# Optimization experiments

Hardware: AMD Instinct MI355X
Metric: run time of the kernel (lower is better)

Reference implementation:

```python
import jax, jax.numpy as jnp
from jax import lax
import numpy as np

EPS_BN = 1e-5
COMMIT = 0.25


def _conv(x, w, b, stride):
    # torch Conv2d(k=3, stride, padding=1); w: (O,I,3,3)
    y = lax.conv_general_dilated(x, w, (stride, stride), ((1, 1), (1, 1)),
                                 dimension_numbers=('NCHW', 'OIHW', 'NCHW'))
    return y + b[None, :, None, None]


def _deconv(x, w, b):
    # torch ConvTranspose2d(k=3, stride=2, padding=1, output_padding=1); w: (I,O,3,3)
    wt = jnp.flip(w, (2, 3)).transpose(1, 0, 2, 3)  # -> (O,I,3,3), spatially flipped
    y = lax.conv_general_dilated(x, wt, (1, 1), ((1, 2), (1, 2)),
                                 lhs_dilation=(2, 2),
                                 dimension_numbers=('NCHW', 'OIHW', 'NCHW'))
    return y + b[None, :, None, None]


def _bn(x, g, b, m, v):
    # eval-mode BatchNorm2d over channel dim 1
    scale = g * lax.rsqrt(v + EPS_BN)
    return (x - m[None, :, None, None]) * scale[None, :, None, None] + b[None, :, None, None]


def _lrelu(x):
    return jax.nn.leaky_relu(x, 0.1)


def _vq(z, emb):
    # z: [B,C,H,W]; emb: [K,C]
    z_nhwc = z.transpose(0, 2, 3, 1)
    B, H, W, C = z_nhwc.shape
    K = emb.shape[0]
    f = z_nhwc.reshape(-1, C)  # [N,C]
    # squared euclidean distances [N,K] without materializing differences
    d = (jnp.sum(f * f, axis=1, keepdims=True)
         - 2.0 * (f @ emb.T)
         + jnp.sum(emb * emb, axis=1)[None, :])
    idx = jnp.argmin(d, axis=1)  # [N]
    q = emb[idx].reshape(B, H, W, C)
    e_latent_loss = jnp.mean((lax.stop_gradient(q) - z_nhwc) ** 2)
    q_latent_loss = jnp.mean((q - lax.stop_gradient(z_nhwc)) ** 2)
    loss = q_latent_loss + COMMIT * e_latent_loss
    q_st = z_nhwc + lax.stop_gradient(q - z_nhwc)  # straight-through
    counts = jnp.zeros((K,), f.dtype).at[idx].add(1.0)
    avg_probs = counts / f.shape[0]
    perplexity = jnp.exp(-jnp.sum(avg_probs * jnp.log(avg_probs + 1e-10)))
    return q_st.transpose(0, 3, 1, 2), loss, perplexity


def reference(x, enc_w1, enc_b1, bn1_g, bn1_b, bn1_m, bn1_v,
              enc_w2, enc_b2, bn2_g, bn2_b, bn2_m, bn2_v,
              enc_w3, enc_b3, bn3_g, bn3_b, bn3_m, bn3_v,
              emb,
              dec_w1, dec_b1, dbn1_g, dbn1_b, dbn1_m, dbn1_v,
              dec_w2, dec_b2, dbn2_g, dbn2_b, dbn2_m, dbn2_v,
              dec_w3, dec_b3):
    # encoder
    h = _lrelu(_bn(_conv(x, enc_w1, enc_b1, 2), bn1_g, bn1_b, bn1_m, bn1_v))
    h = _lrelu(_bn(_conv(h, enc_w2, enc_b2, 2), bn2_g, bn2_b, bn2_m, bn2_v))
    z = _bn(_conv(h, enc_w3, enc_b3, 1), bn3_g, bn3_b, bn3_m, bn3_v)
    # vector quantization
    z_q, vq_loss, perplexity = _vq(z, emb)
    # decoder
    h = _lrelu(_bn(_deconv(z_q, dec_w1, dec_b1), dbn1_g, dbn1_b, dbn1_m, dbn1_v))
    h = _lrelu(_bn(_deconv(h, dec_w2, dec_b2), dbn2_g, dbn2_b, dbn2_m, dbn2_v))
    x_recon = jax.nn.sigmoid(_conv(h, dec_w3, dec_b3, 1))
    return (x_recon, vq_loss, perplexity)


def setup_inputs() -> dict:
    key = jax.random.key(0)
    ks = jax.random.split(key, 10)
    B, Hh, Ww = 32, 256, 256
    C_lat, K = 10, 256
    s = 0.05
    d = {
        'x': jax.random.normal(ks[0], (B, 3, Hh, Ww), jnp.float32),
        'enc_w1': jax.random.normal(ks[1], (32, 3, 3, 3), jnp.float32) * s,
        'enc_b1': jnp.zeros((32,), jnp.float32),
        'bn1_g': jnp.ones((32,), jnp.float32), 'bn1_b': jnp.zeros((32,), jnp.float32),
        'bn1_m': jnp.zeros((32,), jnp.float32), 'bn1_v': jnp.ones((32,), jnp.float32),
        'enc_w2': jax.random.normal(ks[2], (64, 32, 3, 3), jnp.float32) * s,
        'enc_b2': jnp.zeros((64,), jnp.float32),
        'bn2_g': jnp.ones((64,), jnp.float32), 'bn2_b': jnp.zeros((64,), jnp.float32),
        'bn2_m': jnp.zeros((64,), jnp.float32), 'bn2_v': jnp.ones((64,), jnp.float32),
        'enc_w3': jax.random.normal(ks[3], (C_lat, 64, 3, 3), jnp.float32) * s,
        'enc_b3': jnp.zeros((C_lat,), jnp.float32),
        'bn3_g': jnp.ones((C_lat,), jnp.float32), 'bn3_b': jnp.zeros((C_lat,), jnp.float32),
        'bn3_m': jnp.zeros((C_lat,), jnp.float32), 'bn3_v': jnp.ones((C_lat,), jnp.float32),
        'emb': jax.random.uniform(ks[4], (K, C_lat), jnp.float32, -1.0, 1.0),
        'dec_w1': jax.random.normal(ks[5], (C_lat, 64, 3, 3), jnp.float32) * s,
        'dec_b1': jnp.zeros((64,), jnp.float32),
        'dbn1_g': jnp.ones((64,), jnp.float32), 'dbn1_b': jnp.zeros((64,), jnp.float32),
        'dbn1_m': jnp.zeros((64,), jnp.float32), 'dbn1_v': jnp.ones((64,), jnp.float32),
        'dec_w2': jax.random.normal(ks[6], (64, 32, 3, 3), jnp.float32) * s,
        'dec_b2': jnp.zeros((32,), jnp.float32),
        'dbn2_g': jnp.ones((32,), jnp.float32), 'dbn2_b': jnp.zeros((32,), jnp.float32),
        'dbn2_m': jnp.zeros((32,), jnp.float32), 'dbn2_v': jnp.ones((32,), jnp.float32),
        'dec_w3': jax.random.normal(ks[7], (3, 32, 3, 3), jnp.float32) * s,
        'dec_b3': jnp.zeros((3,), jnp.float32),
    }
    return d
```

## Files before the change

### kernel.cpp

```cpp
#include <hip/hip_runtime.h>
#include <hip/hip_bf16.h>
#include <math.h>

typedef __attribute__((ext_vector_type(8))) short bf8v;
typedef __attribute__((ext_vector_type(4))) float f4v;
typedef const __hip_bfloat16* cbfp;

__device__ __forceinline__ void ld4f(const float* p, float* o) {
    float4 t = *(const float4*)p; o[0] = t.x; o[1] = t.y; o[2] = t.z; o[3] = t.w;
}

__global__ __launch_bounds__(256, 2)
void conv1_k(const float* __restrict__ x, const float* __restrict__ w,
             const float* __restrict__ bconv,
             const float* __restrict__ bg, const float* __restrict__ bb,
             const float* __restrict__ bm, const float* __restrict__ bv,
             __hip_bfloat16* __restrict__ out)
{
    __shared__ float sw[3 * 8 * 12];
    int b  = blockIdx.x;
    int yt = b & 15;
    int cg = (b >> 4) & 3;
    int n  = b >> 6;
    int co0 = cg * 8;
    int tid = threadIdx.x;
    for (int idx = tid; idx < 3 * 8 * 9; idx += 256) {
        int t = idx % 9; int rest = idx / 9;
        int cot = rest % 8; int ci = rest / 8;
        sw[(ci * 8 + cot) * 12 + t] = w[(((size_t)(co0 + cot) * 3) + ci) * 9 + t];
    }
    __syncthreads();

    int tx = tid & 31, ty = tid >> 5;
    int y  = yt * 8 + ty;
    int x0 = tx * 4;
    int iyb = 2 * y - 1;
    int ixb = 2 * x0 - 1;

    float acc[8][4];
    #pragma unroll
    for (int c = 0; c < 8; ++c)
        #pragma unroll
        for (int u = 0; u < 4; ++u) acc[c][u] = 0.f;

    for (int ci = 0; ci < 3; ++ci) {
        const float* ipc = x + ((size_t)n * 3 + ci) * 65536;
        float iv[3][9];
        #pragma unroll
        for (int r = 0; r < 3; ++r) {
            int iy = iyb + r;
            bool vy = (unsigned)iy < 256u;
            const float* row = ipc + (size_t)iy * 256;
            if (vy) {
                iv[r][0] = (ixb >= 0) ? row[ixb] : 0.f;
                ld4f(row + ixb + 1, &iv[r][1]);
                ld4f(row + ixb + 5, &iv[r][5]);
            } else {
                #pragma unroll
                for (int c = 0; c < 9; ++c) iv[r][c] = 0.f;
            }
        }
        #pragma unroll
        for (int cot = 0; cot < 8; ++cot) {
            const float4* wp4 = reinterpret_cast<const float4*>(&sw[(ci * 8 + cot) * 12]);
            float4 wa = wp4[0], wb = wp4[1], wc4 = wp4[2];
            float wreg[9] = {wa.x, wa.y, wa.z, wa.w, wb.x, wb.y, wb.z, wb.w, wc4.x};
            #pragma unroll
            for (int r = 0; r < 3; ++r)
                #pragma unroll
                for (int c = 0; c < 3; ++c)
                    #pragma unroll
                    for (int u = 0; u < 4; ++u)
                        acc[cot][u] = fmaf(iv[r][u * 2 + c], wreg[r * 3 + c], acc[cot][u]);
        }
    }

    float rs[8][4];
    #pragma unroll
    for (int cot = 0; cot < 8; ++cot) {
        int co = co0 + cot;
        float s = bg[co] * rsqrtf(bv[co] + 1e-5f);
        float bias = (bconv[co] - bm[co]) * s + bb[co];
        #pragma unroll
        for (int u = 0; u < 4; ++u) {
            float v = acc[cot][u] * s + bias;
            rs[cot][u] = (v >= 0.f) ? v : 0.1f * v;
        }
    }
    #pragma unroll
    for (int u = 0; u < 4; ++u) {
        union { __hip_bfloat162 h[4]; float4 f; } pk;
        #pragma unroll
        for (int p2 = 0; p2 < 4; ++p2)
            pk.h[p2] = __halves2bfloat162(__float2bfloat16(rs[2 * p2][u]),
                                          __float2bfloat16(rs[2 * p2 + 1][u]));
        *(float4*)(out + (((size_t)n * 128 + y) * 128 + (x0 + u)) * 32 + co0) = pk.f;
    }
}

__global__ __launch_bounds__(256)
void pack_conv2_k(const float* __restrict__ w, __hip_bfloat16* __restrict__ bp)
{
    int idx = blockIdx.x * 256 + threadIdx.x;
    if (idx >= 4 * 9 * 64) return;
    int lane = idx & 63;
    int g    = (idx >> 6) % 9;
    int nt   = idx / 576;
    int co   = nt * 16 + (lane & 15);
    __hip_bfloat16* o = bp + (size_t)idx * 8;
    for (int j = 0; j < 8; ++j) {
        int ci = (lane >> 4) * 8 + j;
        o[j] = __float2bfloat16(w[((size_t)co * 32 + ci) * 9 + g]);
    }
}

__global__ __launch_bounds__(256)
void pack_conv3_k(const float* __restrict__ w, __hip_bfloat16* __restrict__ bp)
{
    int idx = blockIdx.x * 256 + threadIdx.x;
    if (idx >= 18 * 64) return;
    int lane = idx & 63;
    int g    = idx >> 6;
    int tap  = g >> 1, cib = g & 1;
    int co   = lane & 15;
    __hip_bfloat16* o = bp + (size_t)idx * 8;
    for (int j = 0; j < 8; ++j) {
        int ci = cib * 32 + (lane >> 4) * 8 + j;
        float f = (co < 10) ? w[((size_t)co * 64 + ci) * 9 + tap] : 0.f;
        o[j] = __float2bfloat16(f);
    }
}

struct DTab { int di[18]; int dj[18]; int wi[18]; int ci0[18]; int ph[18]; };
constexpr DTab TAB1 = {
    {0, 0,0, 1,0, 1,1,0,0,  0,0,0,0,0,0,0,0,0},
    {0, 1,0, 0,0, 1,0,1,0,  0,0,0,0,0,0,0,0,0},
    {4, 3,5, 1,7, 0,2,6,8,  0,0,0,0,0,0,0,0,0},
    {0, 0,0, 0,0, 0,0,0,0,  0,0,0,0,0,0,0,0,0},
    {0, 1,1, 2,2, 3,3,3,3,  0,0,0,0,0,0,0,0,0}};
constexpr DTab TAB2 = {
    {0,0,  0,0,0,0,  1,1,0,0,  1,1,1,1,0,0,0,0},
    {0,0,  1,1,0,0,  0,0,0,0,  1,1,0,0,1,1,0,0},
    {4,4,  3,3,5,5,  1,1,7,7,  0,0,2,2,6,6,8,8},
    {0,32, 0,32,0,32, 0,32,0,32, 0,32,0,32,0,32,0,32},
    {0,0,  1,1,1,1,  2,2,2,2,  3,3,3,3,3,3,3,3}};

template<int WHICH>
__global__ __launch_bounds__(256)
void pack_deconv_k(const float* __restrict__ w, __hip_bfloat16* __restrict__ bp)
{
    constexpr int NKS  = (WHICH == 1) ? 9 : 18;
    constexpr int COUT = (WHICH == 1) ? 64 : 32;
    constexpr int CINr = (WHICH == 1) ? 10 : 64;
    constexpr int NT   = COUT / 16;
    constexpr const DTab& T = (WHICH == 1) ? TAB1 : TAB2;
    int idx = blockIdx.x * 256 + threadIdx.x;
    if (idx >= NT * NKS * 64) return;
    int lane = idx & 63;
    int g    = (idx >> 6) % NKS;
    int nt   = idx / (64 * NKS);
    int co   = nt * 16 + (lane & 15);
    int wi   = T.wi[g], ci0 = T.ci0[g];
    __hip_bfloat16* o = bp + (size_t)idx * 8;
    for (int j = 0; j < 8; ++j) {
        int ci = ci0 + (lane >> 4) * 8 + j;
        float f = (ci < CINr) ? w[((size_t)ci * COUT + co) * 9 + wi] : 0.f;
        o[j] = __float2bfloat16(f);
    }
}

__global__ __launch_bounds__(256)
void pack_convout_k(const float* __restrict__ w, __hip_bfloat16* __restrict__ bp)
{
    int idx = blockIdx.x * 256 + threadIdx.x;
    if (idx >= 9 * 64) return;
    int lane = idx & 63;
    int g    = idx >> 6;
    int co   = lane & 15;
    __hip_bfloat16* o = bp + (size_t)idx * 8;
    for (int j = 0; j < 8; ++j) {
        int ci = (lane >> 4) * 8 + j;
        float f = (co < 3) ? w[((size_t)co * 32 + ci) * 9 + g] : 0.f;
        o[j] = __float2bfloat16(f);
    }
}

__global__ __launch_bounds__(256, 2)
void conv2_mfma_k(const __hip_bfloat16* __restrict__ in,
                  const __hip_bfloat16* __restrict__ bpack,
                  const float* __restrict__ bconv,
                  const float* __restrict__ bg, const float* __restrict__ bb,
                  const float* __restrict__ bm, const float* __restrict__ bv,
                  __hip_bfloat16* __restrict__ out,
                  cbfp zp)
{
    int lane = threadIdx.x & 63;
    int gw = blockIdx.x * 4 + (threadIdx.x >> 6);
    int nt = gw & 3;
    int xt = (gw >> 2) & 3;
    int yt = (gw >> 4) & 15;
    int n  = gw >> 8;
    int m = lane & 15, kc = lane >> 4;
    int xm = xt * 16 + m;

    bf8v bfrag[9];
    const bf8v* bpv = reinterpret_cast<const bf8v*>(bpack);
    #pragma unroll
    for (int g = 0; g < 9; ++g) bfrag[g] = bpv[((size_t)nt * 9 + g) * 64 + lane];

    int co0 = nt * 16 + kc * 4;
    float s4[4], b4[4];
    #pragma unroll
    for (int r = 0; r < 4; ++r) {
        int co = co0 + r;
        float s = bg[co] * rsqrtf(bv[co] + 1e-5f);
        s4[r] = s; b4[r] = (bconv[co] - bm[co]) * s + bb[co];
    }
    bool vc0 = (xm > 0);

    for (int t = 0; t < 4; ++t) {
        int y = yt * 4 + t;
        cbfp rb[3], pc0[3];
        #pragma unroll
        for (int r = 0; r < 3; ++r) {
            int iy = 2 * y + r - 1;
            bool vy = (unsigned)iy < 128u;
            rb[r]  = vy ? in + (((size_t)n * 128 + iy) * 128 + 2 * xm) * 32 + kc * 8 : zp;
            pc0[r] = vc0 ? rb[r] - 32 : zp;
        }
        bf8v av[9];
        #pragma unroll
        for (int g = 0; g < 9; ++g) {
            int r = g / 3, c = g % 3;
            cbfp pg = (c == 0) ? pc0[r] : rb[r];
            av[g] = *reinterpret_cast<const bf8v*>(pg + (c == 2 ? 32 : 0));
        }
        f4v acc = {0, 0, 0, 0};
        #pragma unroll
        for (int g = 0; g < 9; ++g)
            acc = __builtin_amdgcn_mfma_f32_16x16x32_bf16(bfrag[g], av[g], acc, 0, 0, 0);

        union { __hip_bfloat162 h[2]; float2 f; } pk;
        float v0 = acc[0] * s4[0] + b4[0]; v0 = v0 >= 0.f ? v0 : 0.1f * v0;
        float v1 = acc[1] * s4[1] + b4[1]; v1 = v1 >= 0.f ? v1 : 0.1f * v1;
        float v2 = acc[2] * s4[2] + b4[2]; v2 = v2 >= 0.f ? v2 : 0.1f * v2;
        float v3 = acc[3] * s4[3] + b4[3]; v3 = v3 >= 0.f ? v3 : 0.1f * v3;
        pk.h[0] = __halves2bfloat162(__float2bfloat16(v0), __float2bfloat16(v1));
        pk.h[1] = __halves2bfloat162(__float2bfloat16(v2), __float2bfloat16(v3));
        *(float2*)(out + (((size_t)n * 64 + y) * 64 + xm) * 64 + co0) = pk.f;
    }
}

__global__ __launch_bounds__(256, 2)
void conv3_mfma_k(const __hip_bfloat16* __restrict__ in,
                  const __hip_bfloat16* __restrict__ bpack,
                  const float* __restrict__ bconv,
                  const float* __restrict__ bg, const float* __restrict__ bb,
                  const float* __restrict__ bm, const float* __restrict__ bv,
                  float* __restrict__ z, cbfp zp)
{
    __shared__ bf8v sB[18 * 64];
    const bf8v* bpv = reinterpret_cast<const bf8v*>(bpack);
    for (int idx = threadIdx.x; idx < 18 * 64; idx += 256) sB[idx] = bpv[idx];
    __syncthreads();

    int lane = threadIdx.x & 63;
    int gw = blockIdx.x * 4 + (threadIdx.x >> 6);
    int xt = gw & 3;
    int yt = (gw >> 2) & 15;
    int n  = gw >> 6;
    int m = lane & 15, kc = lane >> 4;
    int xm = xt * 16 + m;

    float s4[4], b4[4];
    #pragma unroll
    for (int r = 0; r < 4; ++r) {
        int co = kc * 4 + r;
        if (co < 10) {
            float s = bg[co] * rsqrtf(bv[co] + 1e-5f);
            s4[r] = s; b4[r] = (bconv[co] - bm[co]) * s + bb[co];
        } else { s4[r] = 0.f; b4[r] = 0.f; }
    }
    bool vc0 = (xm > 0), vc2 = (xm < 63);

    for (int t = 0; t < 4; ++t) {
        int y = yt * 4 + t;
        cbfp rb[3], pc0[3], pc2[3];
        #pragma unroll
        for (int r = 0; r < 3; ++r) {
            int iy = y + r - 1;
            bool vy = (unsigned)iy < 64u;
            rb[r]  = vy ? in + (((size_t)n * 64 + iy) * 64 + xm) * 64 + kc * 8 : zp;
            pc0[r] = vc0 ? rb[r] - 64 : zp;
            pc2[r] = vc2 ? rb[r] + 64 : zp;
        }
        bf8v av[18];
        #pragma unroll
        for (int g = 0; g < 18; ++g) {
            int tap = g >> 1, cib = g & 1;
            int r = tap / 3, c = tap % 3;
            cbfp pg = (c == 0) ? pc0[r] : ((c == 2) ? pc2[r] : rb[r]);
            av[g] = *reinterpret_cast<const bf8v*>(pg + cib * 32);
        }
        f4v acc = {0, 0, 0, 0};
        #pragma unroll
        for (int g = 0; g < 18; ++g)
            acc = __builtin_amdgcn_mfma_f32_16x16x32_bf16(sB[g * 64 + lane], av[g], acc, 0, 0, 0);

        #pragma unroll
        for (int r = 0; r < 4; ++r) {
            int co = kc * 4 + r;
            if (co < 10)
                z[(((size_t)n * 10 + co) << 12) + y * 64 + xm] = acc[r] * s4[r] + b4[r];
        }
    }
}

template<int WHICH, int I_T>
__global__ __launch_bounds__(256, 2)
void deconv_mfma_k(const __hip_bfloat16* __restrict__ in,
                   const __hip_bfloat16* __restrict__ bpack,
                   const float* __restrict__ bconv,
                   const float* __restrict__ bg, const float* __restrict__ bb,
                   const float* __restrict__ bm, const float* __restrict__ bv,
                   __hip_bfloat16* __restrict__ out, cbfp zp)
{
    constexpr int NKS  = (WHICH == 1) ? 9 : 18;
    constexpr int CINP = (WHICH == 1) ? 32 : 64;
    constexpr int COUT = (WHICH == 1) ? 64 : 32;
    constexpr int NT   = COUT / 16;
    constexpr int HI   = (WHICH == 1) ? 64 : 128;
    constexpr int HO   = HI * 2;
    constexpr int JT   = HI / 16;
    constexpr const DTab& T = (WHICH == 1) ? TAB1 : TAB2;

    __shared__ bf8v sB[(WHICH == 2) ? NKS * 64 : 1];
    const bf8v* bpv = reinterpret_cast<const bf8v*>(bpack);

    int lane = threadIdx.x & 63;
    int nt, jt, it, n;
    if constexpr (WHICH == 2) {
        nt = blockIdx.x & 1;
        int sid = (blockIdx.x >> 1) * 4 + (threadIdx.x >> 6);
        jt = sid % JT;  sid /= JT;
        it = sid % (HI / I_T);
        n  = sid / (HI / I_T);
        for (int idx = threadIdx.x; idx < NKS * 64; idx += 256)
            sB[idx] = bpv[(size_t)nt * NKS * 64 + idx];
        __syncthreads();
    } else {
        int gw = blockIdx.x * 4 + (threadIdx.x >> 6);
        nt = gw % NT;  int mt = gw / NT;
        jt = mt % JT;  mt /= JT;
        it = mt % (HI / I_T);
        n  = mt / (HI / I_T);
    }
    int j0 = jt * 16;
    int m  = lane & 15, kc = lane >> 4;
    int jm = j0 + m;

    bf8v bfrag[(WHICH == 1) ? NKS : 1];
    if constexpr (WHICH == 1) {
        #pragma unroll
        for (int g = 0; g < NKS; ++g) bfrag[g] = bpv[((size_t)nt * NKS + g) * 64 + lane];
    }

    int co0 = nt * 16 + kc * 4;
    float s4[4], b4[4];
    #pragma unroll
    for (int r = 0; r < 4; ++r) {
        int co = co0 + r;
        float s = bg[co] * rsqrtf(bv[co] + 1e-5f);
        s4[r] = s; b4[r] = (bconv[co] - bm[co]) * s + bb[co];
    }
    bool vj = (jm + 1) < HI;

    for (int t = 0; t < I_T; ++t) {
        int i = it * I_T + t;
        bool vi = (i + 1) < HI;
        cbfp p00 = in + (((size_t)n * HI + i) * HI + jm) * CINP + kc * 8;
        cbfp p01 = vj ? p00 + CINP : zp;
        cbfp p10 = vi ? p00 + (size_t)HI * CINP : zp;
        cbfp p11 = (vi && vj) ? p00 + (size_t)(HI + 1) * CINP : zp;

        bf8v av[NKS];
        #pragma unroll
        for (int g = 0; g < NKS; ++g) {
            cbfp pg = T.di[g] ? (T.dj[g] ? p11 : p10) : (T.dj[g] ? p01 : p00);
            av[g] = *reinterpret_cast<const bf8v*>(pg + T.ci0[g]);
        }
        f4v acc[4] = {{0,0,0,0},{0,0,0,0},{0,0,0,0},{0,0,0,0}};
        #pragma unroll
        for (int g = 0; g < NKS; ++g) {
            bf8v bw;
            if constexpr (WHICH == 2) bw = sB[g * 64 + lane];
            else                      bw = bfrag[g];
            acc[T.ph[g]] = __builtin_amdgcn_mfma_f32_16x16x32_bf16(bw, av[g], acc[T.ph[g]], 0, 0, 0);
        }

        __hip_bfloat16* ob = out + (((size_t)n * HO + 2 * i) * HO + 2 * jm) * COUT + co0;
        #pragma unroll
        for (int p = 0; p < 4; ++p) {
            int py = p >> 1, px = p & 1;
            float v0 = acc[p][0] * s4[0] + b4[0]; v0 = v0 >= 0.f ? v0 : 0.1f * v0;
            float v1 = acc[p][1] * s4[1] + b4[1]; v1 = v1 >= 0.f ? v1 : 0.1f * v1;
            float v2 = acc[p][2] * s4[2] + b4[2]; v2 = v2 >= 0.f ? v2 : 0.1f * v2;
            float v3 = acc[p][3] * s4[3] + b4[3]; v3 = v3 >= 0.f ? v3 : 0.1f * v3;
            union { __hip_bfloat162 h[2]; float2 f; } pk;
            pk.h[0] = __halves2bfloat162(__float2bfloat16(v0), __float2bfloat16(v1));
            pk.h[1] = __halves2bfloat162(__float2bfloat16(v2), __float2bfloat16(v3));
            *(float2*)(ob + ((size_t)py * HO + px) * COUT) = pk.f;
        }
    }
}

__global__ __launch_bounds__(256, 2)
void convout_mfma_k(const __hip_bfloat16* __restrict__ in,
                    const __hip_bfloat16* __restrict__ bpack,
                    const float* __restrict__ b3,
                    float* __restrict__ out, cbfp zp)
{
    int lane = threadIdx.x & 63;
    int gw = blockIdx.x * 4 + (threadIdx.x >> 6);
    int xt = gw & 15;
    int yt = (gw >> 4) & 63;
    int n  = gw >> 10;
    int m = lane & 15, kc = lane >> 4;
    int xm = xt * 16 + m;

    bf8v bfrag[9];
    #pragma unroll
    for (int g = 0; g < 9; ++g)
        bfrag[g] = reinterpret_cast<const bf8v*>(bpack)[g * 64 + lane];

    float bias0 = b3[0], bias1 = b3[1], bias2 = b3[2];
    bool vc0 = (xm > 0), vc2 = (xm < 255);

    for (int t = 0; t < 4; ++t) {
        int y = yt * 4 + t;
        cbfp rb[3], pc0[3], pc2[3];
        #pragma unroll
        for (int r = 0; r < 3; ++r) {
            int iy = y + r - 1;
            bool vy = (unsigned)iy < 256u;
            rb[r]  = vy ? in + (((size_t)n * 256 + iy) * 256 + xm) * 32 + kc * 8 : zp;
            pc0[r] = vc0 ? rb[r] - 32 : zp;
            pc2[r] = vc2 ? rb[r] + 32 : zp;
        }
        bf8v av[9];
        #pragma unroll
        for (int g = 0; g < 9; ++g) {
            int r = g / 3, c = g % 3;
            cbfp pg = (c == 0) ? pc0[r] : ((c == 2) ? pc2[r] : rb[r]);
            av[g] = *reinterpret_cast<const bf8v*>(pg);
        }
        f4v acc = {0, 0, 0, 0};
        #pragma unroll
        for (int g = 0; g < 9; ++g)
            acc = __builtin_amdgcn_mfma_f32_16x16x32_bf16(bfrag[g], av[g], acc, 0, 0, 0);

        if (kc == 0) {
            size_t ybase = ((size_t)n * 3) * 65536 + (size_t)y * 256 + xm;
            float v0 = acc[0] + bias0;
            float v1 = acc[1] + bias1;
            float v2 = acc[2] + bias2;
            out[ybase]             = 1.f / (1.f + __expf(-v0));
            out[ybase + 65536]     = 1.f / (1.f + __expf(-v1));
            out[ybase + 131072]    = 1.f / (1.f + __expf(-v2));
        }
    }
}

__global__ __launch_bounds__(256)
void vq_k(const float* __restrict__ z, const float* __restrict__ emb,
          __hip_bfloat16* __restrict__ q, float* __restrict__ sse_acc,
          unsigned int* __restrict__ counts, int HW, int CHW)
{
    __shared__ float se[256 * 10];
    __shared__ unsigned int hist[256];
    __shared__ float wsum[4];
    int tid = threadIdx.x;
    for (int i = tid; i < 2560; i += 256) se[i] = emb[i];
    hist[tid] = 0u;
    __syncthreads();

    int pos = blockIdx.x * 256 + tid;
    int b = pos / HW;
    int sp = pos - b * HW;
    const float* zpz = z + (size_t)b * CHW + sp;
    float zv[10];
    #pragma unroll
    for (int c = 0; c < 10; ++c) zv[c] = zpz[(size_t)c * HW];

    float best = 3.4e38f;
    int bi = 0;
    for (int k = 0; k < 256; ++k) {
        const float* e = se + k * 10;
        float d = 0.f;
        #pragma unroll
        for (int c = 0; c < 10; ++c) { float t = zv[c] - e[c]; d = fmaf(t, t, d); }
        if (d < best) { best = d; bi = k; }
    }
    atomicAdd(&hist[bi], 1u);

    __hip_bfloat16* qp = q + (size_t)pos * 32;
    float lsse = 0.f;
    #pragma unroll
    for (int c = 0; c < 10; ++c) {
        float e = se[bi * 10 + c];
        qp[c] = __float2bfloat16(e);
        float t = e - zv[c];
        lsse = fmaf(t, t, lsse);
    }
    #pragma unroll
    for (int c = 10; c < 32; ++c) qp[c] = __float2bfloat16(0.f);

    #pragma unroll
    for (int off = 32; off > 0; off >>= 1) lsse += __shfl_down(lsse, off, 64);
    if ((tid & 63) == 0) wsum[tid >> 6] = lsse;
    __syncthreads();
    if (tid == 0) atomicAdd(sse_acc, wsum[0] + wsum[1] + wsum[2] + wsum[3]);
    atomicAdd(&counts[tid], hist[tid]);
}

__global__ __launch_bounds__(256)
void vq_finalize_k(const float* __restrict__ sse_acc, const unsigned int* __restrict__ counts,
                   float* __restrict__ out_loss, float* __restrict__ out_ppl,
                   float invNC, float invN)
{
    __shared__ float w4[4];
    int tid = threadIdx.x;
    float p = (float)counts[tid] * invN;
    float t = p * logf(p + 1e-10f);
    #pragma unroll
    for (int off = 32; off > 0; off >>= 1) t += __shfl_down(t, off, 64);
    if ((tid & 63) == 0) w4[tid >> 6] = t;
    __syncthreads();
    if (tid == 0) {
        float s = w4[0] + w4[1] + w4[2] + w4[3];
        *out_ppl  = expf(-s);
        *out_loss = 1.25f * sse_acc[0] * invNC;
    }
}

__global__ void zero_k(float* p, int n) {
    int i = blockIdx.x * 256 + threadIdx.x;
    if (i < n) p[i] = 0.f;
}

extern "C" void kernel_launch(void* const* d_in, const int* in_sizes, int n_in,
                              void* d_out, int out_size, void* d_ws, size_t ws_size,
                              hipStream_t stream) {
    const float* x      = (const float*)d_in[0];
    const float* enc_w1 = (const float*)d_in[1];
    const float* enc_b1 = (const float*)d_in[2];
    const float* bn1_g  = (const float*)d_in[3];
    const float* bn1_b  = (const float*)d_in[4];
    const float* bn1_m  = (const float*)d_in[5];
    const float* bn1_v  = (const float*)d_in[6];
    const float* enc_w2 = (const float*)d_in[7];
    const float* enc_b2 = (const float*)d_in[8];
    const float* bn2_g  = (const float*)d_in[9];
    const float* bn2_b  = (const float*)d_in[10];
    const float* bn2_m  = (const float*)d_in[11];
    const float* bn2_v  = (const float*)d_in[12];
    const float* enc_w3 = (const float*)d_in[13];
    const float* enc_b3 = (const float*)d_in[14];
    const float* bn3_g  = (const float*)d_in[15];
    const float* bn3_b  = (const float*)d_in[16];
    const float* bn3_m  = (const float*)d_in[17];
    const float* bn3_v  = (const float*)d_in[18];
    const float* emb    = (const float*)d_in[19];
    const float* dec_w1 = (const float*)d_in[20];
    const float* dec_b1 = (const float*)d_in[21];
    const float* dbn1_g = (const float*)d_in[22];
    const float* dbn1_b = (const float*)d_in[23];
    const float* dbn1_m = (const float*)d_in[24];
    const float* dbn1_v = (const float*)d_in[25];
    const float* dec_w2 = (const float*)d_in[26];
    const float* dec_b2 = (const float*)d_in[27];
    const float* dbn2_g = (const float*)d_in[28];
    const float* dbn2_b = (const float*)d_in[29];
    const float* dbn2_m = (const float*)d_in[30];
    const float* dbn2_v = (const float*)d_in[31];
    const float* dec_w3 = (const float*)d_in[32];
    const float* dec_b3 = (const float*)d_in[33];

    float* ws = (float*)d_ws;
    const size_t SSE_OFF  = 0;
    const size_t CNT_OFF  = 4;
    const size_t ZP_OFF   = 260;
    const size_t BPC2_OFF = 516;
    const size_t BPC3_OFF = 9732;
    const size_t BP1_OFF  = 14340;
    const size_t BP2_OFF  = 23556;
    const size_t BPO_OFF  = 32772;
    const size_t Q_OFF    = 35076;
    const size_t Z_OFF    = 2132228;
    const size_t H1_OFF   = 3442948;
    const size_t H2_OFF   = 11831556;
    const size_t DD2_OFF  = 2132228;
    const size_t DD1_OFF  = 18909444;
    const size_t NEEDED_F = DD1_OFF + 16777216;

    if (ws_size < NEEDED_F * sizeof(float)) return;

    float* sse  = ws + SSE_OFF;
    unsigned int* counts = (unsigned int*)(ws + CNT_OFF);
    cbfp zp = (cbfp)(ws + ZP_OFF + 128);
    __hip_bfloat16* bpc2 = (__hip_bfloat16*)(ws + BPC2_OFF);
    __hip_bfloat16* bpc3 = (__hip_bfloat16*)(ws + BPC3_OFF);
    __hip_bfloat16* bp1  = (__hip_bfloat16*)(ws + BP1_OFF);
    __hip_bfloat16* bp2  = (__hip_bfloat16*)(ws + BP2_OFF);
    __hip_bfloat16* bpo  = (__hip_bfloat16*)(ws + BPO_OFF);
    __hip_bfloat16* qbuf = (__hip_bfloat16*)(ws + Q_OFF);
    float* zbuf = ws + Z_OFF;
    __hip_bfloat16* h1  = (__hip_bfloat16*)(ws + H1_OFF);
    __hip_bfloat16* h2  = (__hip_bfloat16*)(ws + H2_OFF);
    __hip_bfloat16* dd1 = (__hip_bfloat16*)(ws + DD1_OFF);
    __hip_bfloat16* dd2 = (__hip_bfloat16*)(ws + DD2_OFF);
    float* out = (float*)d_out;

    zero_k<<<3, 256, 0, stream>>>(ws, 516);
    pack_conv2_k<<<9, 256, 0, stream>>>(enc_w2, bpc2);
    pack_conv3_k<<<5, 256, 0, stream>>>(enc_w3, bpc3);
    pack_deconv_k<1><<<9, 256, 0, stream>>>(dec_w1, bp1);
    pack_deconv_k<2><<<9, 256, 0, stream>>>(dec_w2, bp2);
    pack_convout_k<<<3, 256, 0, stream>>>(dec_w3, bpo);

    conv1_k<<<2048, 256, 0, stream>>>(x, enc_w1, enc_b1, bn1_g, bn1_b, bn1_m, bn1_v, h1);
    conv2_mfma_k<<<2048, 256, 0, stream>>>(h1, bpc2, enc_b2, bn2_g, bn2_b, bn2_m, bn2_v, h2, zp);
    conv3_mfma_k<<<512, 256, 0, stream>>>(h2, bpc3, enc_b3, bn3_g, bn3_b, bn3_m, bn3_v, zbuf, zp);

    vq_k<<<512, 256, 0, stream>>>(zbuf, emb, qbuf, sse, counts, 4096, 40960);

    deconv_mfma_k<1, 2><<<4096, 256, 0, stream>>>(
        qbuf, bp1, dec_b1, dbn1_g, dbn1_b, dbn1_m, dbn1_v, dd1, zp);
    deconv_mfma_k<2, 2><<<8192, 256, 0, stream>>>(
        dd1, bp2, dec_b2, dbn2_g, dbn2_b, dbn2_m, dbn2_v, dd2, zp);
    convout_mfma_k<<<8192, 256, 0, stream>>>(dd2, bpo, dec_b3, out, zp);

    vq_finalize_k<<<1, 256, 0, stream>>>(sse, counts, out + 6291456, out + 6291457,
                                         1.f / 1310720.f, 1.f / 131072.f);
}
```

Measured before the change: 469.6 us.

## Use 16-channel planar intermediate layout and split decoder tail into batch halves

Decoder intermediates dd1 and dd2 are now stored as planes of 16 channels rather than interleaved full-channel rows, and the reading kernels compute per-plane addresses. The second deconv and the output conv now run in two launches over half the batch each, so dd2 only holds 16 images at a time. The aim is to keep that intermediate small enough to stay resident in cache between producer and consumer, and to make accesses more contiguous. The cost is extra launches and more complex addressing.

```diff
diff --git a/kernel.cpp b/kernel.cpp
--- a/kernel.cpp
+++ b/kernel.cpp
@@ -323,28 +323,30 @@
                    const float* __restrict__ bconv,
                    const float* __restrict__ bg, const float* __restrict__ bb,
                    const float* __restrict__ bm, const float* __restrict__ bv,
-                   __hip_bfloat16* __restrict__ out, cbfp zp)
+                   __hip_bfloat16* __restrict__ out, cbfp zp, int n_base)
 {
     constexpr int NKS  = (WHICH == 1) ? 9 : 18;
-    constexpr int CINP = (WHICH == 1) ? 32 : 64;
     constexpr int COUT = (WHICH == 1) ? 64 : 32;
     constexpr int NT   = COUT / 16;
     constexpr int HI   = (WHICH == 1) ? 64 : 128;
     constexpr int HO   = HI * 2;
     constexpr int JT   = HI / 16;
+    constexpr size_t PL_IN  = (size_t)32 * 128 * 128 * 16;
+    constexpr size_t PL_OUT = (WHICH == 1) ? (size_t)32 * 128 * 128 * 16
+                                           : (size_t)16 * 256 * 256 * 16;
     constexpr const DTab& T = (WHICH == 1) ? TAB1 : TAB2;
 
     __shared__ bf8v sB[(WHICH == 2) ? NKS * 64 : 1];
     const bf8v* bpv = reinterpret_cast<const bf8v*>(bpack);
 
     int lane = threadIdx.x & 63;
-    int nt, jt, it, n;
+    int nt, jt, it, nl;
     if constexpr (WHICH == 2) {
         nt = blockIdx.x & 1;
         int sid = (blockIdx.x >> 1) * 4 + (threadIdx.x >> 6);
         jt = sid % JT;  sid /= JT;
         it = sid % (HI / I_T);
-        n  = sid / (HI / I_T);
+        nl = sid / (HI / I_T);
         for (int idx = threadIdx.x; idx < NKS * 64; idx += 256)
             sB[idx] = bpv[(size_t)nt * NKS * 64 + idx];
         __syncthreads();
@@ -353,8 +355,9 @@
         nt = gw % NT;  int mt = gw / NT;
         jt = mt % JT;  mt /= JT;
         it = mt % (HI / I_T);
-        n  = mt / (HI / I_T);
-    }
+        nl = mt / (HI / I_T);
+    }
+    int n = n_base + nl;
     int j0 = jt * 16;
     int m  = lane & 15, kc = lane >> 4;
     int jm = j0 + m;
@@ -378,17 +381,37 @@
     for (int t = 0; t < I_T; ++t) {
         int i = it * I_T + t;
         bool vi = (i + 1) < HI;
-        cbfp p00 = in + (((size_t)n * HI + i) * HI + jm) * CINP + kc * 8;
-        cbfp p01 = vj ? p00 + CINP : zp;
-        cbfp p10 = vi ? p00 + (size_t)HI * CINP : zp;
-        cbfp p11 = (vi && vj) ? p00 + (size_t)(HI + 1) * CINP : zp;
-
         bf8v av[NKS];
-        #pragma unroll
-        for (int g = 0; g < NKS; ++g) {
-            cbfp pg = T.di[g] ? (T.dj[g] ? p11 : p10) : (T.dj[g] ? p01 : p00);
-            av[g] = *reinterpret_cast<const bf8v*>(pg + T.ci0[g]);
-        }
+
+        if constexpr (WHICH == 1) {
+            cbfp p00 = in + (((size_t)n * HI + i) * HI + jm) * 32 + kc * 8;
+            cbfp p01 = vj ? p00 + 32 : zp;
+            cbfp p10 = vi ? p00 + (size_t)HI * 32 : zp;
+            cbfp p11 = (vi && vj) ? p00 + (size_t)(HI + 1) * 32 : zp;
+            #pragma unroll
+            for (int g = 0; g < NKS; ++g) {
+                cbfp pg = T.di[g] ? (T.dj[g] ? p11 : p10) : (T.dj[g] ? p01 : p00);
+                av[g] = *reinterpret_cast<const bf8v*>(pg);
+            }
+        } else {
+            cbfp baseA = in + (size_t)(kc >> 1) * PL_IN + (kc & 1) * 8;
+            cbfp pA00 = baseA + (((size_t)n * HI + i) * HI + jm) * 16;
+            cbfp pB00 = pA00 + 2 * PL_IN;
+            cbfp pA01 = vj ? pA00 + 16 : zp;
+            cbfp pB01 = vj ? pB00 + 16 : zp;
+            cbfp pA10 = vi ? pA00 + (size_t)HI * 16 : zp;
+            cbfp pB10 = vi ? pB00 + (size_t)HI * 16 : zp;
+            cbfp pA11 = (vi && vj) ? pA00 + (size_t)(HI + 1) * 16 : zp;
+            cbfp pB11 = (vi && vj) ? pB00 + (size_t)(HI + 1) * 16 : zp;
+            #pragma unroll
+            for (int g = 0; g < NKS; ++g) {
+                cbfp pg;
+                if (T.ci0[g]) pg = T.di[g] ? (T.dj[g] ? pB11 : pB10) : (T.dj[g] ? pB01 : pB00);
+                else          pg = T.di[g] ? (T.dj[g] ? pA11 : pA10) : (T.dj[g] ? pA01 : pA00);
+                av[g] = *reinterpret_cast<const bf8v*>(pg);
+            }
+        }
+
         f4v acc[4] = {{0,0,0,0},{0,0,0,0},{0,0,0,0},{0,0,0,0}};
         #pragma unroll
         for (int g = 0; g < NKS; ++g) {
@@ -398,7 +421,8 @@
             acc[T.ph[g]] = __builtin_amdgcn_mfma_f32_16x16x32_bf16(bw, av[g], acc[T.ph[g]], 0, 0, 0);
         }
 
-        __hip_bfloat16* ob = out + (((size_t)n * HO + 2 * i) * HO + 2 * jm) * COUT + co0;
+        __hip_bfloat16* ob = out + (size_t)nt * PL_OUT
+                           + (((size_t)nl * HO + 2 * i) * HO + 2 * jm) * 16 + kc * 4;
         #pragma unroll
         for (int p = 0; p < 4; ++p) {
             int py = p >> 1, px = p & 1;
@@ -409,7 +433,7 @@
             union { __hip_bfloat162 h[2]; float2 f; } pk;
             pk.h[0] = __halves2bfloat162(__float2bfloat16(v0), __float2bfloat16(v1));
             pk.h[1] = __halves2bfloat162(__float2bfloat16(v2), __float2bfloat16(v3));
-            *(float2*)(ob + ((size_t)py * HO + px) * COUT) = pk.f;
+            *(float2*)(ob + ((size_t)py * HO + px) * 16) = pk.f;
         }
     }
 }
@@ -418,13 +442,15 @@
 void convout_mfma_k(const __hip_bfloat16* __restrict__ in,
                     const __hip_bfloat16* __restrict__ bpack,
                     const float* __restrict__ b3,
-                    float* __restrict__ out, cbfp zp)
-{
+                    float* __restrict__ out, cbfp zp, int n_base)
+{
+    constexpr size_t PL2 = (size_t)16 * 256 * 256 * 16;
     int lane = threadIdx.x & 63;
     int gw = blockIdx.x * 4 + (threadIdx.x >> 6);
     int xt = gw & 15;
     int yt = (gw >> 4) & 63;
-    int n  = gw >> 10;
+    int nl = gw >> 10;
+    int n  = n_base + nl;
     int m = lane & 15, kc = lane >> 4;
     int xm = xt * 16 + m;
 
@@ -435,6 +461,7 @@
 
     float bias0 = b3[0], bias1 = b3[1], bias2 = b3[2];
     bool vc0 = (xm > 0), vc2 = (xm < 255);
+    cbfp baseA = in + (size_t)(kc >> 1) * PL2 + (kc & 1) * 8;
 
     for (int t = 0; t < 4; ++t) {
         int y = yt * 4 + t;
@@ -443,9 +470,9 @@
         for (int r = 0; r < 3; ++r) {
             int iy = y + r - 1;
             bool vy = (unsigned)iy < 256u;
-            rb[r]  = vy ? in + (((size_t)n * 256 + iy) * 256 + xm) * 32 + kc * 8 : zp;
-            pc0[r] = vc0 ? rb[r] - 32 : zp;
-            pc2[r] = vc2 ? rb[r] + 32 : zp;
+            rb[r]  = vy ? baseA + (((size_t)nl * 256 + iy) * 256 + xm) * 16 : zp;
+            pc0[r] = vc0 ? rb[r] - 16 : zp;
+            pc2[r] = vc2 ? rb[r] + 16 : zp;
         }
         bf8v av[9];
         #pragma unroll
@@ -635,10 +662,12 @@
     vq_k<<<512, 256, 0, stream>>>(zbuf, emb, qbuf, sse, counts, 4096, 40960);
 
     deconv_mfma_k<1, 2><<<4096, 256, 0, stream>>>(
-        qbuf, bp1, dec_b1, dbn1_g, dbn1_b, dbn1_m, dbn1_v, dd1, zp);
-    deconv_mfma_k<2, 2><<<8192, 256, 0, stream>>>(
-        dd1, bp2, dec_b2, dbn2_g, dbn2_b, dbn2_m, dbn2_v, dd2, zp);
-    convout_mfma_k<<<8192, 256, 0, stream>>>(dd2, bpo, dec_b3, out, zp);
+        qbuf, bp1, dec_b1, dbn1_g, dbn1_b, dbn1_m, dbn1_v, dd1, zp, 0);
+    for (int half = 0; half < 2; ++half) {
+        deconv_mfma_k<2, 2><<<4096, 256, 0, stream>>>(
+            dd1, bp2, dec_b2, dbn2_g, dbn2_b, dbn2_m, dbn2_v, dd2, zp, half * 16);
+        convout_mfma_k<<<4096, 256, 0, stream>>>(dd2, bpo, dec_b3, out, zp, half * 16);
+    }
 
     vq_finalize_k<<<1, 256, 0, stream>>>(sse, counts, out + 6291456, out + 6291457,
                                          1.f / 1310720.f, 1.f / 131072.f);
```

New measurement: 447.4 us. 4.7% less time.
